# Kernel optimization log

Measured on AMD Instinct MI355X. Metric: run time of the kernel, lower is better.

## Reference

```python
import jax, jax.numpy as jnp
from jax import lax
import numpy as np

IOU_THRESHOLD = 0.35
SCORE_THRESHOLD = 0.5


def _pairwise_iou(b):
    # b: [N,4] boxes in (ymin, xmin, ymax, xmax) convention (tf boxes)
    y1, x1, y2, x2 = b[:, 0], b[:, 1], b[:, 2], b[:, 3]
    area = (y2 - y1) * (x2 - x1)
    iy1 = jnp.maximum(y1[:, None], y1[None, :])
    ix1 = jnp.maximum(x1[:, None], x1[None, :])
    iy2 = jnp.minimum(y2[:, None], y2[None, :])
    ix2 = jnp.minimum(x2[:, None], x2[None, :])
    inter = jnp.maximum(iy2 - iy1, 0.0) * jnp.maximum(ix2 - ix1, 0.0)
    union = area[:, None] + area[None, :] - inter
    return jnp.where(union > 0, inter / union, 0.0)  # [N,N]


def _nms_sample_image(scores, boxes, anchors_wh, num_samples):
    # scores [N], boxes [N,4], anchors_wh [N,2]
    N = scores.shape[0]
    order = jnp.argsort(-scores)  # descending by score, like tf NMS
    s = scores[order]
    b = boxes[order]
    a = anchors_wh[order]
    valid = s > SCORE_THRESHOLD
    iou = _pairwise_iou(b)  # [N,N] on score-sorted boxes
    idx = jnp.arange(N)

    # greedy suppression: box i kept iff valid and no earlier kept box overlaps > thr
    def step(keep, i):
        suppressed = jnp.any(keep & (idx < i) & (iou[i] > IOU_THRESHOLD))
        return keep.at[i].set(valid[i] & ~suppressed), None

    keep, _ = lax.scan(step, jnp.zeros(N, dtype=bool), idx)

    # gather kept entries in (descending-score) order, then pad/slice to num_samples
    rank = jnp.cumsum(keep) - 1  # output slot for each kept entry
    slot = jnp.where(keep, jnp.minimum(rank, num_samples), num_samples)
    vals = jnp.concatenate([s[:, None], b, a], axis=1)  # [N,7]
    out = jnp.zeros((num_samples + 1, 7), vals.dtype).at[slot].set(vals)
    return out[:num_samples]  # [num_samples, 7] = (score | box(4) | anchor_wh(2))


def reference(scores, boxes, anchors, num_samples):
    # scores [B,H,W,1], boxes [B,H,W,4], anchors [B,H,W,4] (last 2 chans = w,h)
    B = scores.shape[0]
    sc = scores.reshape(B, -1)
    bx = boxes.reshape(B, -1, 4)
    an = anchors[..., 2:].reshape(B, -1, 2)
    out = jax.vmap(lambda s, b, a: _nms_sample_image(s, b, a, num_samples))(sc, bx, an)
    return out  # [B, num_samples, 7]


def setup_inputs() -> dict:
    key = jax.random.key(0)
    k1, k2, k3, k4, k5 = jax.random.split(key, 5)
    B, H, W = 8, 64, 64
    scores = jax.random.uniform(k1, (B, H, W, 1), dtype=jnp.float32)
    # well-formed tf boxes: ymin<ymax, xmin<xmax in [0,1]
    ymin = jax.random.uniform(k2, (B, H, W, 1), dtype=jnp.float32) * 0.8
    xmin = jax.random.uniform(k3, (B, H, W, 1), dtype=jnp.float32) * 0.8
    hh = jax.random.uniform(k4, (B, H, W, 1), dtype=jnp.float32) * 0.18 + 0.02
    ww = jax.random.uniform(k5, (B, H, W, 1), dtype=jnp.float32) * 0.18 + 0.02
    boxes = jnp.concatenate([ymin, xmin, ymin + hh, xmin + ww], axis=-1)
    # anchors: [cy, cx, w, h]-style; only last two channels are used
    k6 = jax.random.fold_in(key, 6)
    anchors = jax.random.uniform(k6, (B, H, W, 4), dtype=jnp.float32) * 0.25 + 0.05
    return {"scores": scores, "boxes": boxes, "anchors": anchors, "num_samples": 300}
```

## Files before the change

kernel.cpp:

```cpp
#include <hip/hip_runtime.h>

static constexpr float kIouT = 0.35f;
static constexpr float kScoreT = 0.5f;
static constexpr int kMaxKeep = 512;

__device__ __forceinline__ bool iou_gt(const float4 a, const float4 b) {
  const float iy1 = fmaxf(a.x, b.x), ix1 = fmaxf(a.y, b.y);
  const float iy2 = fminf(a.z, b.z), ix2 = fminf(a.w, b.w);
  const float dy = iy2 - iy1, dx = ix2 - ix1;
  if (!(dy > 0.0f && dx > 0.0f)) return false;
  const float inter = __fmul_rn(dy, dx);
  const float aA = __fmul_rn(a.z - a.x, a.w - a.y);
  const float aB = __fmul_rn(b.z - b.x, b.w - b.y);
  const float uni = (aA + aB) - inter;
  return (uni > 0.0f) && (__fdiv_rn(inter, uni) > kIouT);
}

__device__ __forceinline__ unsigned long long rdlane64(unsigned long long v,
                                                       int l) {
  unsigned lo = (unsigned)__builtin_amdgcn_readlane((int)(unsigned)v, l);
  unsigned hi = (unsigned)__builtin_amdgcn_readlane((int)(unsigned)(v >> 32), l);
  return ((unsigned long long)hi << 32) | lo;
}

__global__ __launch_bounds__(256)
void nms_rank_kernel(const float* __restrict__ scores,
                     const float4* __restrict__ boxes,
                     unsigned long long* __restrict__ skeys,
                     float4* __restrict__ sboxes,
                     int* __restrict__ Mcnt, int N, int rankBlocks) {
  const int tid = threadIdx.x;
  const int lane = tid & 63;
  if ((int)blockIdx.x >= rankBlocks) {
    __shared__ int part[4];
    const int img = blockIdx.x - rankBlocks;
    const int wv = tid >> 6;
    const float4* sc4 = (const float4*)(scores + (size_t)img * N);
    int c = 0;
    for (int q = tid; q < (N >> 2); q += 256) {
      float4 v = sc4[q];
      c += (v.x > kScoreT) + (v.y > kScoreT) + (v.z > kScoreT) + (v.w > kScoreT);
    }
#pragma unroll
    for (int off = 1; off < 64; off <<= 1) c += __shfl_xor(c, off, 64);
    if (lane == 0) part[wv] = c;
    __syncthreads();
    if (tid == 0) Mcnt[img] = part[0] + part[1] + part[2] + part[3];
    return;
  }
  const int wid = (int)(((unsigned)blockIdx.x * blockDim.x + tid) >> 6);
  const int img = wid / N;
  const int row = wid - img * N;
  const float* sc = scores + (size_t)img * N;
  const float si = sc[row];
  if (!(si > kScoreT)) return;
  const float4* sc4 = (const float4*)sc;
  int cnt = 0;
  for (int q = lane; q < (N >> 2); q += 64) {
    const float4 v = sc4[q];
    const int j = q << 2;
    cnt += (v.x > si) + (v.y > si) + (v.z > si) + (v.w > si);
    if (v.x == si && j < row) cnt++;
    if (v.y == si && j + 1 < row) cnt++;
    if (v.z == si && j + 2 < row) cnt++;
    if (v.w == si && j + 3 < row) cnt++;
  }
#pragma unroll
  for (int off = 1; off < 64; off <<= 1) cnt += __shfl_xor(cnt, off, 64);
  if (lane == 0) {
    skeys[(size_t)img * N + cnt] =
        ((unsigned long long)(~__float_as_uint(si)) << 32) | (unsigned)row;
    sboxes[(size_t)img * N + cnt] = boxes[(size_t)img * N + row];
  }
}

__global__ __launch_bounds__(256)
void nms_mask_kernel(const float4* __restrict__ sboxes,
                     const int* __restrict__ Mcnt,
                     unsigned long long* __restrict__ mask,
                     int N, int totalRows) {
  const int wid = (int)(((unsigned)blockIdx.x * blockDim.x + threadIdx.x) >> 6);
  const int lane = threadIdx.x & 63;
  if (wid >= totalRows) return;
  const int img = wid / N;
  const int row = wid - img * N;
  const int m = Mcnt[img];
  if (row >= m) return;
  const float4* sb = sboxes + (size_t)img * N;
  const float4 bi = sb[row];
  const int nw = (m + 63) >> 6;
  unsigned long long* mrow = mask + (size_t)wid * (size_t)(N >> 6);
  for (int w = row >> 6; w < nw; ++w) {
    int j = (w << 6) | lane;
    bool sup = false;
    if (j > row && j < m) sup = iou_gt(bi, sb[j]);
    unsigned long long bm = __ballot(sup);
    if (lane == 0) __builtin_nontemporal_store(bm, &mrow[w]);
  }
}

__global__ __launch_bounds__(64, 1)
void nms_scan_kernel(const unsigned long long* __restrict__ skeys,
                     const float4* __restrict__ sboxes,
                     const int* __restrict__ Mcnt,
                     const unsigned long long* __restrict__ mask,
                     const float* __restrict__ anchors,
                     float* __restrict__ out, int N, int NS) {
  __shared__ int keptlist[kMaxKeep];
  const int img = blockIdx.x;
  const int lane = threadIdx.x;
  int m = Mcnt[img];
  if (m > N) m = N;
  if (m < 0) m = 0;
  const int nw = (m + 63) >> 6;
  const int stride = N >> 6;
  const unsigned long long* mbase = mask + (size_t)img * (size_t)N * stride;
  const unsigned long long* kg = skeys + (size_t)img * N;
  const float4* sb = sboxes + (size_t)img * N;
  const float* an = anchors + (size_t)img * (size_t)N * 4;
  float* o = out + (size_t)img * NS * 7;

  int kept = 0;
  unsigned long long remv = 0ull;

  if (m > 0) {
    auto dgload = [&](int cc) -> unsigned long long {
      const int cl = cc < (nw - 1) ? cc : (nw - 1);
      return __builtin_nontemporal_load(
          &mbase[(size_t)((cl << 6) + lane) * stride + cl]);
    };
    unsigned long long dg0 = dgload(0);
    unsigned long long dg1 = dgload(1);
    unsigned long long dg2 = dgload(2);

    for (int c = 0; c < nw && kept < NS; ++c) {
      const int cb = c << 6;
      unsigned long long local = rdlane64(remv, c);
      const int rem = m - cb;
      unsigned long long avail = ~local;
      if (rem < 64) avail &= (1ull << rem) - 1ull;
      unsigned long long keptbits = 0ull;
      const int keptbase = kept;
      while (avail != 0ull && kept < NS) {
        const int b = (int)__builtin_ctzll(avail);
        keptbits |= 1ull << b;
        kept++;
        const unsigned long long rc = rdlane64(dg0, b);
        local |= rc;
        avail &= ~local;
        avail &= ~(1ull << b);
      }
      dg0 = dg1; dg1 = dg2; dg2 = dgload(c + 3);
      if (keptbits != 0ull) {
        if (lane == 0) {
          unsigned long long kl = keptbits;
          int kc = keptbase;
          while (kl != 0ull) {
            const int b = (int)__builtin_ctzll(kl);
            kl &= kl - 1ull;
            keptlist[kc++] = cb + b;
          }
        }
        if (kept < NS || c + 1 < nw) {
          const bool lok = (lane > c) && (lane < nw);
          unsigned long long kb = keptbits;
          while (kb != 0ull) {
            int bs[16];
            int bcur = (int)__builtin_ctzll(kb);
#pragma unroll
            for (int k = 0; k < 16; ++k) {
              if (kb != 0ull) {
                bcur = (int)__builtin_ctzll(kb);
                kb &= kb - 1ull;
              }
              bs[k] = bcur;
            }
            unsigned long long t[16];
#pragma unroll
            for (int k = 0; k < 16; ++k)
              t[k] = __builtin_nontemporal_load(
                  &mbase[(size_t)(cb + bs[k]) * stride + lane]);
            unsigned long long acc = 0ull;
#pragma unroll
            for (int k = 0; k < 16; ++k) acc |= t[k];
            if (lok) remv |= acc;
          }
        }
      }
    }
  }

  __syncthreads();
  for (int t = lane; t < kept; t += 64) {
    const int i = keptlist[t];
    const unsigned long long ki = kg[i];
    const float4 bi = sb[i];
    const unsigned idx = (unsigned)ki;
    float* row = o + t * 7;
    row[0] = __uint_as_float(~(unsigned)(ki >> 32));
    row[1] = bi.x; row[2] = bi.y; row[3] = bi.z; row[4] = bi.w;
    row[5] = an[idx * 4 + 2];
    row[6] = an[idx * 4 + 3];
  }
  for (int t = kept * 7 + lane; t < NS * 7; t += 64) o[t] = 0.0f;
}

__global__ __launch_bounds__(1024)
void nms_fused_kernel(const float* __restrict__ scores,
                      const float4* __restrict__ boxes,
                      const float* __restrict__ anchors,
                      float* __restrict__ out, int N, int NS) {
  __shared__ unsigned long long keys[4096];
  __shared__ int s_m;
  if (N > 4096) return;
  const int img = blockIdx.x;
  const int tid = threadIdx.x;
  const float* sc = scores + (size_t)img * N;
  const float4* bx = boxes + (size_t)img * N;
  if (tid == 0) s_m = 0;
  __syncthreads();
  int cnt = 0;
  for (int i = tid; i < N; i += blockDim.x) {
    float s = sc[i];
    keys[i] = ((unsigned long long)(~__float_as_uint(s)) << 32) | (unsigned)i;
    if (s > kScoreT) cnt++;
  }
  if (cnt) atomicAdd(&s_m, cnt);
  __syncthreads();
  for (int k = 2; k <= N; k <<= 1) {
    for (int j = k >> 1; j > 0; j >>= 1) {
      for (int i = tid; i < N; i += blockDim.x) {
        int ixj = i ^ j;
        if (ixj > i) {
          unsigned long long a = keys[i];
          unsigned long long b = keys[ixj];
          bool up = ((i & k) == 0);
          if (up ? (a > b) : (a < b)) { keys[i] = b; keys[ixj] = a; }
        }
      }
      __syncthreads();
    }
  }
  if (tid >= 64) return;
  const int lane = tid;
  const int m = s_m;
  const int nw = (m + 63) >> 6;
  const float* an = anchors + (size_t)img * N * 4;
  float* o = out + (size_t)img * NS * 7;
  unsigned long long remv = 0ull;
  int kept = 0;
  for (int i = 0; i < m && kept < NS; ++i) {
    unsigned long long rw = __shfl(remv, i >> 6, 64);
    if ((rw >> (i & 63)) & 1ull) continue;
    unsigned long long ki = keys[i];
    float4 bi = bx[(unsigned)ki];
    if (lane == 0) {
      unsigned idx = (unsigned)ki;
      float* row = o + kept * 7;
      row[0] = __uint_as_float(~(unsigned)(ki >> 32));
      row[1] = bi.x; row[2] = bi.y; row[3] = bi.z; row[4] = bi.w;
      row[5] = an[idx * 4 + 2];
      row[6] = an[idx * 4 + 3];
    }
    kept++;
    for (int w2 = i >> 6; w2 < nw; ++w2) {
      int j = (w2 << 6) | lane;
      bool sup = false;
      if (j > i && j < m) sup = iou_gt(bi, bx[(unsigned)keys[j]]);
      unsigned long long bm = __ballot(sup);
      if (lane == w2) remv |= bm;
    }
  }
  for (int t = kept * 7 + lane; t < NS * 7; t += 64) o[t] = 0.0f;
}

extern "C" void kernel_launch(void* const* d_in, const int* in_sizes, int n_in,
                              void* d_out, int out_size, void* d_ws, size_t ws_size,
                              hipStream_t stream) {
  const float* scores = (const float*)d_in[0];
  const float4* boxes = (const float4*)d_in[1];
  const float* anchors = (const float*)d_in[2];
  float* out = (float*)d_out;
  const int B = 8;
  const int N = in_sizes[0] / B;
  const int NS = out_size / (B * 7);

  const size_t nTot = (size_t)B * (size_t)N;
  const size_t keysB = nTot * 8;
  const size_t sboxB = nTot * 16;
  const size_t mcntB = 256;
  const size_t maskB = nTot * (size_t)(N >> 6) * 8;
  const size_t need = keysB + sboxB + mcntB + maskB;

  if (ws_size >= need && (N % 256) == 0 && N >= 256 && N <= 4096 &&
      NS <= kMaxKeep) {
    char* p = (char*)d_ws;
    unsigned long long* skeys = (unsigned long long*)p; p += keysB;
    float4* sboxes = (float4*)p;                         p += sboxB;
    int* Mcnt = (int*)p;                                 p += mcntB;
    unsigned long long* mask = (unsigned long long*)p;

    const int totalRows = B * N;
    const int rankBlocks = totalRows / 4;
    nms_rank_kernel<<<rankBlocks + B, 256, 0, stream>>>(scores, boxes, skeys,
                                                        sboxes, Mcnt, N,
                                                        rankBlocks);
    nms_mask_kernel<<<rankBlocks, 256, 0, stream>>>(sboxes, Mcnt, mask, N,
                                                    totalRows);
    nms_scan_kernel<<<B, 64, 0, stream>>>(skeys, sboxes, Mcnt, mask, anchors,
                                          out, N, NS);
  } else {
    nms_fused_kernel<<<B, 1024, 0, stream>>>(scores, boxes, anchors, out, N, NS);
  }
}
```

Before: 101.8 us.

## Transpose suppression mask and keep column blocks in registers during scan

After: 150.3 us. 1.48x slower.

```diff
diff --git a/kernel.cpp b/kernel.cpp
--- a/kernel.cpp
+++ b/kernel.cpp
@@ -3,6 +3,7 @@
 static constexpr float kIouT = 0.35f;
 static constexpr float kScoreT = 0.5f;
 static constexpr int kMaxKeep = 512;
+static constexpr int kNW = 36;
 
 __device__ __forceinline__ bool iou_gt(const float4 a, const float4 b) {
   const float iy1 = fmaxf(a.x, b.x), ix1 = fmaxf(a.y, b.y);
@@ -75,10 +76,10 @@
 }
 
 __global__ __launch_bounds__(256)
-void nms_mask_kernel(const float4* __restrict__ sboxes,
-                     const int* __restrict__ Mcnt,
-                     unsigned long long* __restrict__ mask,
-                     int N, int totalRows) {
+void nms_maskT_kernel(const float4* __restrict__ sboxes,
+                      const int* __restrict__ Mcnt,
+                      unsigned long long* __restrict__ maskT,
+                      int N, int totalRows) {
   const int wid = (int)(((unsigned)blockIdx.x * blockDim.x + threadIdx.x) >> 6);
   const int lane = threadIdx.x & 63;
   if (wid >= totalRows) return;
@@ -88,24 +89,68 @@
   if (row >= m) return;
   const float4* sb = sboxes + (size_t)img * N;
   const float4 bi = sb[row];
-  const int nw = (m + 63) >> 6;
-  unsigned long long* mrow = mask + (size_t)wid * (size_t)(N >> 6);
-  for (int w = row >> 6; w < nw; ++w) {
-    int j = (w << 6) | lane;
-    bool sup = false;
-    if (j > row && j < m) sup = iou_gt(bi, sb[j]);
-    unsigned long long bm = __ballot(sup);
-    if (lane == 0) __builtin_nontemporal_store(bm, &mrow[w]);
-  }
-}
+  const int rc = row >> 6;
+  unsigned long long* base = maskT + (size_t)img * (size_t)(N >> 6) * N;
+  for (int w = 0; w <= rc; ++w) {
+    const int j = (w << 6) | lane;
+    const bool sup = (j < row) && iou_gt(bi, sb[j]);
+    const unsigned long long bm = __ballot(sup);
+    if (lane == 0) base[(size_t)w * N + row] = bm;
+  }
+}
+
+#define SCAN_BODY(CVAR, CUR, NXT)                                              \
+  {                                                                            \
+    const int c_ = (CVAR);                                                     \
+    const int cb_ = c_ << 6;                                                   \
+    _Pragma("unroll") for (int k = 0; k < kNW; ++k) {                          \
+      if (k > c_ && k < nw)                                                    \
+        NXT[k] = base[(size_t)(c_ + 1) * N + (k << 6) + lane];                 \
+    }                                                                          \
+    unsigned long long diagw = 0ull;                                           \
+    _Pragma("unroll") for (int k = 0; k < kNW; ++k) {                          \
+      if (k == c_) diagw = CUR[k];                                             \
+    }                                                                          \
+    const bool mysup = ((supfut >> c_) & 1ull) != 0ull;                        \
+    unsigned long long avail = ~__ballot(mysup);                               \
+    const int rem_ = m - cb_;                                                  \
+    if (rem_ < 64) avail &= (1ull << rem_) - 1ull;                             \
+    unsigned long long keptbits = 0ull;                                        \
+    const int keptbase = kept;                                                 \
+    while (avail != 0ull && kept < NS) {                                       \
+      const int b = (int)__builtin_ctzll(avail);                               \
+      keptbits |= 1ull << b;                                                   \
+      kept++;                                                                  \
+      const bool sb2 = ((diagw >> b) & 1ull) != 0ull;                          \
+      const unsigned long long rc2 = __ballot(sb2);                            \
+      avail &= ~rc2;                                                           \
+      avail &= ~(1ull << b);                                                   \
+    }                                                                          \
+    if (lane == 0 && keptbits != 0ull) {                                       \
+      unsigned long long kl = keptbits;                                        \
+      int kc = keptbase;                                                       \
+      while (kl != 0ull) {                                                     \
+        const int b = (int)__builtin_ctzll(kl);                                \
+        kl &= kl - 1ull;                                                       \
+        keptlist[kc++] = cb_ + b;                                              \
+      }                                                                        \
+    }                                                                          \
+    if (keptbits != 0ull) {                                                    \
+      _Pragma("unroll") for (int k = 0; k < kNW; ++k) {                        \
+        if (k > c_ && k < nw) {                                                \
+          if ((CUR[k] & keptbits) != 0ull) supfut |= 1ull << k;                \
+        }                                                                      \
+      }                                                                        \
+    }                                                                          \
+  }
 
 __global__ __launch_bounds__(64, 1)
-void nms_scan_kernel(const unsigned long long* __restrict__ skeys,
-                     const float4* __restrict__ sboxes,
-                     const int* __restrict__ Mcnt,
-                     const unsigned long long* __restrict__ mask,
-                     const float* __restrict__ anchors,
-                     float* __restrict__ out, int N, int NS) {
+void nms_scanT_kernel(const unsigned long long* __restrict__ skeys,
+                      const float4* __restrict__ sboxes,
+                      const int* __restrict__ Mcnt,
+                      const unsigned long long* __restrict__ maskT,
+                      const float* __restrict__ anchors,
+                      float* __restrict__ out, int N, int NS) {
   __shared__ int keptlist[kMaxKeep];
   const int img = blockIdx.x;
   const int lane = threadIdx.x;
@@ -113,79 +158,40 @@
   if (m > N) m = N;
   if (m < 0) m = 0;
   const int nw = (m + 63) >> 6;
-  const int stride = N >> 6;
-  const unsigned long long* mbase = mask + (size_t)img * (size_t)N * stride;
+  const unsigned long long* base =
+      maskT + (size_t)img * (size_t)(N >> 6) * N;
   const unsigned long long* kg = skeys + (size_t)img * N;
   const float4* sb = sboxes + (size_t)img * N;
   const float* an = anchors + (size_t)img * (size_t)N * 4;
   float* o = out + (size_t)img * NS * 7;
 
   int kept = 0;
-  unsigned long long remv = 0ull;
-
-  if (m > 0) {
-    auto dgload = [&](int cc) -> unsigned long long {
-      const int cl = cc < (nw - 1) ? cc : (nw - 1);
-      return __builtin_nontemporal_load(
-          &mbase[(size_t)((cl << 6) + lane) * stride + cl]);
-    };
-    unsigned long long dg0 = dgload(0);
-    unsigned long long dg1 = dgload(1);
-    unsigned long long dg2 = dgload(2);
-
-    for (int c = 0; c < nw && kept < NS; ++c) {
-      const int cb = c << 6;
-      unsigned long long local = rdlane64(remv, c);
-      const int rem = m - cb;
-      unsigned long long avail = ~local;
-      if (rem < 64) avail &= (1ull << rem) - 1ull;
-      unsigned long long keptbits = 0ull;
-      const int keptbase = kept;
-      while (avail != 0ull && kept < NS) {
-        const int b = (int)__builtin_ctzll(avail);
-        keptbits |= 1ull << b;
-        kept++;
-        const unsigned long long rc = rdlane64(dg0, b);
-        local |= rc;
-        avail &= ~local;
-        avail &= ~(1ull << b);
-      }
-      dg0 = dg1; dg1 = dg2; dg2 = dgload(c + 3);
-      if (keptbits != 0ull) {
-        if (lane == 0) {
-          unsigned long long kl = keptbits;
-          int kc = keptbase;
-          while (kl != 0ull) {
-            const int b = (int)__builtin_ctzll(kl);
-            kl &= kl - 1ull;
-            keptlist[kc++] = cb + b;
-          }
-        }
-        if (kept < NS || c + 1 < nw) {
-          const bool lok = (lane > c) && (lane < nw);
-          unsigned long long kb = keptbits;
-          while (kb != 0ull) {
-            int bs[16];
-            int bcur = (int)__builtin_ctzll(kb);
+  if (m > 0 && nw <= kNW) {
+    unsigned long long colA[kNW], colB[kNW];
+    unsigned long long supfut = 0ull;
 #pragma unroll
-            for (int k = 0; k < 16; ++k) {
-              if (kb != 0ull) {
-                bcur = (int)__builtin_ctzll(kb);
-                kb &= kb - 1ull;
-              }
-              bs[k] = bcur;
-            }
-            unsigned long long t[16];
-#pragma unroll
-            for (int k = 0; k < 16; ++k)
-              t[k] = __builtin_nontemporal_load(
-                  &mbase[(size_t)(cb + bs[k]) * stride + lane]);
-            unsigned long long acc = 0ull;
-#pragma unroll
-            for (int k = 0; k < 16; ++k) acc |= t[k];
-            if (lok) remv |= acc;
-          }
-        }
+    for (int k = 0; k < kNW; ++k)
+      colA[k] = (k < nw) ? base[(size_t)0 * N + (k << 6) + lane] : 0ull;
+    for (int c = 0; c < nw && kept < NS;) {
+      SCAN_BODY(c, colA, colB);
+      ++c;
+      if (c >= nw || kept >= NS) break;
+      SCAN_BODY(c, colB, colA);
+      ++c;
+    }
+  } else if (m > 0) {
+    unsigned long long remv = 0ull;
+    for (int i = 0; i < m && kept < NS; ++i) {
+      const unsigned long long rw = rdlane64(remv, i >> 6);
+      if ((rw >> (i & 63)) & 1ull) continue;
+      if (lane == 0) keptlist[kept] = i;
+      kept++;
+      const float4 bi = sb[i];
+      for (int w2 = i >> 6; w2 < nw; ++w2) {
+        const int j = (w2 << 6) | lane;
+        const bool sup = (j > i) && (j < m) && iou_gt(bi, sb[j]);
+        const unsigned long long bm = __ballot(sup);
+        remv |= (lane == w2) ? bm : 0ull;
       }
     }
   }
@@ -298,17 +304,17 @@
     unsigned long long* skeys = (unsigned long long*)p; p += keysB;
     float4* sboxes = (float4*)p;                         p += sboxB;
     int* Mcnt = (int*)p;                                 p += mcntB;
-    unsigned long long* mask = (unsigned long long*)p;
+    unsigned long long* maskT = (unsigned long long*)p;
 
     const int totalRows = B * N;
     const int rankBlocks = totalRows / 4;
     nms_rank_kernel<<<rankBlocks + B, 256, 0, stream>>>(scores, boxes, skeys,
                                                         sboxes, Mcnt, N,
                                                         rankBlocks);
-    nms_mask_kernel<<<rankBlocks, 256, 0, stream>>>(sboxes, Mcnt, mask, N,
-                                                    totalRows);
-    nms_scan_kernel<<<B, 64, 0, stream>>>(skeys, sboxes, Mcnt, mask, anchors,
-                                          out, N, NS);
+    nms_maskT_kernel<<<rankBlocks, 256, 0, stream>>>(sboxes, Mcnt, maskT, N,
+                                                     totalRows);
+    nms_scanT_kernel<<<B, 64, 0, stream>>>(skeys, sboxes, Mcnt, maskT, anchors,
+                                           out, N, NS);
   } else {
     nms_fused_kernel<<<B, 1024, 0, stream>>>(scores, boxes, anchors, out, N, NS);
   }
```
